# Performance work log

Hardware: AMD Instinct MI355X
Metric: run time of the kernel (lower is better)

Reference implementation:

```python
import jax, jax.numpy as jnp
import numpy as np

D_MODEL = 1024
N_HEADS = 16
HEAD_DIM = D_MODEL // N_HEADS


def setup_inputs() -> dict:
    key = jax.random.key(0)
    ks = jax.random.split(key, 6)
    s = 1.0 / np.sqrt(D_MODEL)
    x = jax.random.normal(ks[0], (4, 2048, D_MODEL), dtype=jnp.float32)
    Wq = jax.random.uniform(ks[1], (D_MODEL, D_MODEL), jnp.float32, -s, s)
    Wk = jax.random.uniform(ks[2], (D_MODEL, D_MODEL), jnp.float32, -s, s)
    Wv = jax.random.uniform(ks[3], (D_MODEL, D_MODEL), jnp.float32, -s, s)
    Wo = jax.random.uniform(ks[4], (D_MODEL, D_MODEL), jnp.float32, -s, s)
    bo = jax.random.uniform(ks[5], (D_MODEL,), jnp.float32, -s, s)
    return {"x": x, "Wq": Wq, "Wk": Wk, "Wv": Wv, "Wo": Wo, "bo": bo}


def reference(x, Wq, Wk, Wv, Wo, bo):
    B, S, _ = x.shape
    # nn.Linear: x @ W.T
    def proj(W):
        return (x @ W.T).reshape(B, S, N_HEADS, HEAD_DIM).transpose(0, 2, 1, 3)
    q = proj(Wq)  # [B,H,S,Dh]
    k = proj(Wk)
    v = proj(Wv)
    scores = jnp.einsum("bhqd,bhkd->bhqk", q, k) / jnp.sqrt(jnp.float32(HEAD_DIM))
    attn = jax.nn.softmax(scores, axis=-1)
    out = jnp.einsum("bhqk,bhkd->bhqd", attn, v)
    out = out.transpose(0, 2, 1, 3).reshape(B, S, D_MODEL)
    return out @ Wo.T + bo
```

## Files before the change

### kernel.cpp

```cpp
#include <hip/hip_runtime.h>
#include <hip/hip_bf16.h>
#include <math.h>

#define BB 4
#define SS 2048
#define DM 1024
#define NH 16
#define DH 64
#define MROWS (BB*SS)
#define NT (SS/64)

typedef __attribute__((ext_vector_type(8))) short bf16x8;
typedef __attribute__((ext_vector_type(4))) float f32x4;
typedef __attribute__((ext_vector_type(8))) unsigned short u16x8;

__device__ __forceinline__ unsigned short f2b(float f) {
    __hip_bfloat16 b = __float2bfloat16(f);
    return *reinterpret_cast<unsigned short*>(&b);
}

__device__ __forceinline__ float fexp2(float x) {
    float r;
    asm("v_exp_f32 %0, %1" : "=v"(r) : "v"(x));
    return r;
}

__device__ __forceinline__ void gload_lds16(const void* g, void* l) {
    __builtin_amdgcn_global_load_lds((const __attribute__((address_space(1))) unsigned int*)g,
                                     (__attribute__((address_space(3))) unsigned int*)l,
                                     16, 0, 0);
}

__global__ __launch_bounds__(256) void cast_x_kernel(const float* __restrict__ in,
                                                     unsigned short* __restrict__ out) {
    const size_t i = ((size_t)blockIdx.x * 256 + threadIdx.x) * 8;
    const float4 a = *(const float4*)(in + i);
    const float4 b = *(const float4*)(in + i + 4);
    unsigned short pk[8] = {f2b(a.x), f2b(a.y), f2b(a.z), f2b(a.w),
                            f2b(b.x), f2b(b.y), f2b(b.z), f2b(b.w)};
    *(u16x8*)(out + i) = *(u16x8*)pk;
}

__global__ __launch_bounds__(256) void cast_w_kernel(const float* __restrict__ Wq,
                                                     const float* __restrict__ Wk,
                                                     const float* __restrict__ Wv,
                                                     const float* __restrict__ Wo,
                                                     unsigned short* __restrict__ out) {
    const float* src = (blockIdx.y == 0) ? Wq : (blockIdx.y == 1) ? Wk
                     : (blockIdx.y == 2) ? Wv : Wo;
    const size_t i = ((size_t)blockIdx.x * 256 + threadIdx.x) * 8;
    const float4 a = *(const float4*)(src + i);
    const float4 b = *(const float4*)(src + i + 4);
    unsigned short pk[8] = {f2b(a.x), f2b(a.y), f2b(a.z), f2b(a.w),
                            f2b(b.x), f2b(b.y), f2b(b.z), f2b(b.w)};
    *(u16x8*)(out + (size_t)blockIdx.y * DM * DM + i) = *(u16x8*)pk;
}

template<int MODE>
__global__ __launch_bounds__(256) void gemm_mfma(const unsigned short* __restrict__ A,
                                                 const unsigned short* __restrict__ Wq,
                                                 const unsigned short* __restrict__ Wk,
                                                 const unsigned short* __restrict__ Wv,
                                                 unsigned short* __restrict__ Oq,
                                                 unsigned short* __restrict__ Ok,
                                                 unsigned short* __restrict__ Ov,
                                                 float* __restrict__ outf,
                                                 const float* __restrict__ bias) {
    __shared__ __align__(16) unsigned short As[128 * 64];
    __shared__ __align__(16) unsigned short Bs[128 * 64];
    const int t  = threadIdx.x;
    const int l  = t & 63;
    const int w  = t >> 6;
    const int g  = l >> 4;
    const int cc = l & 15;
    const int wr = w >> 1, wc = w & 1;
    const int m0 = blockIdx.x * 128;
    const int n0 = blockIdx.y * 128;

    const unsigned short* W;
    unsigned short* Ob = nullptr;
    float oscale = 1.f;
    if (MODE == 0) {
        const int z = blockIdx.z;
        W  = (z == 0) ? Wq : (z == 1) ? Wk : Wv;
        Ob = (z == 0) ? Oq : (z == 1) ? Ok : Ov;
        if (z == 0) oscale = 0.18033688011112042f;
    } else {
        W = Wq;
    }

    const f32x4 zf = {0.f, 0.f, 0.f, 0.f};
    f32x4 acc[4][4] = {{zf,zf,zf,zf},{zf,zf,zf,zf},{zf,zf,zf,zf},{zf,zf,zf,zf}};

    for (int k0 = 0; k0 < DM; k0 += 64) {
        __syncthreads();
        #pragma unroll
        for (int i = 0; i < 4; ++i) {
            const int s   = i * 256 + t;
            const int row = s >> 3;
            const int j   = s & 7;
            const int gb  = j ^ (row & 7);
            gload_lds16(A + (size_t)(m0 + row) * DM + k0 + gb * 8, &As[s * 8]);
            gload_lds16(W + (size_t)(n0 + row) * DM + k0 + gb * 8, &Bs[s * 8]);
        }
        asm volatile("s_waitcnt vmcnt(0)" ::: "memory");
        __syncthreads();

        #pragma unroll
        for (int kk = 0; kk < 2; ++kk) {
            bf16x8 af[4], bf[4];
            #pragma unroll
            for (int mi = 0; mi < 4; ++mi) {
                const int row = wr * 64 + mi * 16 + cc;
                const int jb  = (kk * 4 + g) ^ (row & 7);
                af[mi] = *(const bf16x8*)&As[(row * 8 + jb) * 8];
            }
            #pragma unroll
            for (int ni = 0; ni < 4; ++ni) {
                const int row = wc * 64 + ni * 16 + cc;
                const int jb  = (kk * 4 + g) ^ (row & 7);
                bf[ni] = *(const bf16x8*)&Bs[(row * 8 + jb) * 8];
            }
            #pragma unroll
            for (int mi = 0; mi < 4; ++mi)
                #pragma unroll
                for (int ni = 0; ni < 4; ++ni)
                    acc[mi][ni] = __builtin_amdgcn_mfma_f32_16x16x32_bf16(af[mi], bf[ni], acc[mi][ni], 0, 0, 0);
        }
    }

    #pragma unroll
    for (int mi = 0; mi < 4; ++mi) {
        #pragma unroll
        for (int r = 0; r < 4; ++r) {
            const int m = m0 + wr * 64 + mi * 16 + 4 * g + r;
            if (MODE == 0) {
                const int b = m >> 11, s = m & 2047;
                #pragma unroll
                for (int ni = 0; ni < 4; ++ni) {
                    const int col = n0 + wc * 64 + ni * 16 + cc;
                    const int h = col >> 6, dh = col & 63;
                    Ob[((size_t)(b * NH + h) * SS + s) * DH + dh] = f2b(acc[mi][ni][r] * oscale);
                }
            } else {
                #pragma unroll
                for (int ni = 0; ni < 4; ++ni) {
                    const int col = n0 + wc * 64 + ni * 16 + cc;
                    outf[(size_t)m * DM + col] = acc[mi][ni][r] + bias[col];
                }
            }
        }
    }
}

__global__ __launch_bounds__(256) void transpose_v(const unsigned short* __restrict__ Vb,
                                                   unsigned short* __restrict__ Vt) {
    __shared__ unsigned short T[64][72];
    const int t  = threadIdx.x;
    const int bh = blockIdx.y;
    const int s0 = blockIdx.x * 64;
    #pragma unroll
    for (int r = 0; r < 2; ++r) {
        const int idx = t + 256 * r;
        const int row = idx >> 3;
        const int d8  = (idx & 7) * 8;
        *(u16x8*)&T[row][d8] = *(const u16x8*)(Vb + ((size_t)bh * SS + s0 + row) * 64 + d8);
    }
    __syncthreads();
    const int d  = t >> 2;
    const int sc = (t & 3) * 16;
    unsigned short tmp[16];
    #pragma unroll
    for (int i = 0; i < 16; ++i) tmp[i] = T[sc + i][d];
    unsigned short* dst = Vt + ((size_t)bh * 64 + d) * SS + s0 + sc;
    *(u16x8*)(dst)     = *(u16x8*)&tmp[0];
    *(u16x8*)(dst + 8) = *(u16x8*)&tmp[8];
}

__global__ __launch_bounds__(256) void attn_mfma(const unsigned short* __restrict__ Qb,
                                                 const unsigned short* __restrict__ Kb,
                                                 const unsigned short* __restrict__ Vtp,
                                                 unsigned short* __restrict__ AOb) {
    __shared__ __align__(16) unsigned short Ks[2][64*64];
    __shared__ __align__(16) unsigned short Vs[2][64*64];
    __shared__ unsigned short Ps[64*64];
    const int t    = threadIdx.x;
    const int lane = t & 63;
    const int w    = t >> 6;
    const int g    = lane >> 4;
    const int cc   = lane & 15;
    const int bh   = blockIdx.y;
    const int q0   = blockIdx.x * 64;

    const unsigned short* Qw = Qb + ((size_t)bh * SS + q0 + w * 16 + cc) * 64;
    const bf16x8 qf0 = *(const bf16x8*)(Qw + 8 * g);
    const bf16x8 qf1 = *(const bf16x8*)(Qw + 32 + 8 * g);

    const unsigned short* Kbase = Kb  + (size_t)bh * SS * 64;
    const unsigned short* Vbase = Vtp + (size_t)bh * 64 * SS;

    auto stage = [&](int buf, int kt) {
        #pragma unroll
        for (int r2 = 0; r2 < 2; ++r2) {
            const int idx = r2 * 256 + t;
            const int row = idx >> 3;
            const int gb  = (idx & 7) ^ (row & 7);
            gload_lds16(Kbase + (size_t)(kt * 64 + row) * 64 + gb * 8, &Ks[buf][idx * 8]);
            gload_lds16(Vbase + (size_t)row * SS + kt * 64 + gb * 8, &Vs[buf][idx * 8]);
        }
    };

    asm volatile("s_waitcnt vmcnt(0)" ::: "memory");
    stage(0, 0);

    const f32x4 zf = {0.f, 0.f, 0.f, 0.f};
    f32x4 oacc[4] = {zf, zf, zf, zf};
    float mrow[4] = {-INFINITY, -INFINITY, -INFINITY, -INFINITY};
    float lrow[4] = {0.f, 0.f, 0.f, 0.f};

    for (int kt = 0; kt < NT; ++kt) {
        const int cur = kt & 1;
        if (kt + 1 < NT) {
            stage(cur ^ 1, kt + 1);
            asm volatile("s_waitcnt vmcnt(4)" ::: "memory");
        } else {
            asm volatile("s_waitcnt vmcnt(0)" ::: "memory");
        }
        __syncthreads();

        f32x4 sacc[4] = {zf, zf, zf, zf};
        __builtin_amdgcn_s_setprio(1);
        #pragma unroll
        for (int n = 0; n < 4; ++n) {
            const int key = n * 16 + cc;
            const bf16x8 kf0 = *(const bf16x8*)&Ks[cur][key * 64 + ((g       ^ (key & 7)) << 3)];
            const bf16x8 kf1 = *(const bf16x8*)&Ks[cur][key * 64 + (((4 + g) ^ (key & 7)) << 3)];
            sacc[n] = __builtin_amdgcn_mfma_f32_16x16x32_bf16(qf0, kf0, sacc[n], 0, 0, 0);
            sacc[n] = __builtin_amdgcn_mfma_f32_16x16x32_bf16(qf1, kf1, sacc[n], 0, 0, 0);
        }
        __builtin_amdgcn_s_setprio(0);

        float p[4][4];
        float scl[4];
        #pragma unroll
        for (int r = 0; r < 4; ++r) {
            float mx = fmaxf(fmaxf(sacc[0][r], sacc[1][r]), fmaxf(sacc[2][r], sacc[3][r]));
            mx = fmaxf(mx, __shfl_xor(mx, 1));
            mx = fmaxf(mx, __shfl_xor(mx, 2));
            mx = fmaxf(mx, __shfl_xor(mx, 4));
            mx = fmaxf(mx, __shfl_xor(mx, 8));
            const float nm = fmaxf(mrow[r], mx);
            scl[r] = fexp2(mrow[r] - nm);
            mrow[r] = nm;
            float rs = 0.f;
            #pragma unroll
            for (int n = 0; n < 4; ++n) {
                const float pv = fexp2(sacc[n][r] - nm);
                p[n][r] = pv;
                rs += pv;
            }
            rs += __shfl_xor(rs, 1);
            rs += __shfl_xor(rs, 2);
            rs += __shfl_xor(rs, 4);
            rs += __shfl_xor(rs, 8);
            lrow[r] = lrow[r] * scl[r] + rs;
        }

        #pragma unroll
        for (int n = 0; n < 4; ++n)
            #pragma unroll
            for (int r = 0; r < 4; ++r) {
                const int qr  = w * 16 + g * 4 + r;
                const int key = n * 16 + cc;
                Ps[qr * 64 + (key ^ ((qr & 7) << 3))] = f2b(p[n][r]);
            }

        #pragma unroll
        for (int n = 0; n < 4; ++n) {
            oacc[n][0] *= scl[0]; oacc[n][1] *= scl[1];
            oacc[n][2] *= scl[2]; oacc[n][3] *= scl[3];
        }

        const int qrow = w * 16 + cc;
        __builtin_amdgcn_s_setprio(1);
        #pragma unroll
        for (int ks = 0; ks < 2; ++ks) {
            const bf16x8 pf = *(const bf16x8*)&Ps[qrow * 64 + (((ks * 4 + g) ^ (qrow & 7)) << 3)];
            #pragma unroll
            for (int n = 0; n < 4; ++n) {
                const int vrow = n * 16 + cc;
                const bf16x8 vf = *(const bf16x8*)&Vs[cur][vrow * 64 + (((ks * 4 + g) ^ (vrow & 7)) << 3)];
                oacc[n] = __builtin_amdgcn_mfma_f32_16x16x32_bf16(pf, vf, oacc[n], 0, 0, 0);
            }
        }
        __builtin_amdgcn_s_setprio(0);

        __syncthreads();
    }

    const int b = bh >> 4, h = bh & 15;
    #pragma unroll
    for (int r = 0; r < 4; ++r) {
        const float inv  = 1.f / lrow[r];
        const int   srow = q0 + w * 16 + g * 4 + r;
        unsigned short* dst = AOb + ((size_t)(b * SS + srow)) * DM + h * 64;
        dst[ 0 + cc] = f2b(oacc[0][r] * inv);
        dst[16 + cc] = f2b(oacc[1][r] * inv);
        dst[32 + cc] = f2b(oacc[2][r] * inv);
        dst[48 + cc] = f2b(oacc[3][r] * inv);
    }
}

extern "C" void kernel_launch(void* const* d_in, const int* in_sizes, int n_in,
                              void* d_out, int out_size, void* d_ws, size_t ws_size,
                              hipStream_t stream) {
    const float* x  = (const float*)d_in[0];
    const float* Wq = (const float*)d_in[1];
    const float* Wk = (const float*)d_in[2];
    const float* Wv = (const float*)d_in[3];
    const float* Wo = (const float*)d_in[4];
    const float* bo = (const float*)d_in[5];
    float* out = (float*)d_out;

    const size_t NEL = (size_t)MROWS * DM;
    unsigned short* xb  = (unsigned short*)d_ws;
    unsigned short* Wb  = xb + NEL;
    unsigned short* Qb  = Wb + (size_t)4 * DM * DM;
    unsigned short* Kb  = Qb + NEL;
    unsigned short* Vb  = Kb + NEL;
    unsigned short* Vt  = Vb + NEL;
    unsigned short* AOb = Vt + NEL;

    const dim3 blk(256);
    cast_x_kernel<<<dim3(NEL / (256 * 8)), blk, 0, stream>>>(x, xb);
    cast_w_kernel<<<dim3(DM * DM / (256 * 8), 4), blk, 0, stream>>>(Wq, Wk, Wv, Wo, Wb);

    gemm_mfma<0><<<dim3(MROWS / 128, DM / 128, 3), blk, 0, stream>>>(
        xb, Wb, Wb + (size_t)DM * DM, Wb + (size_t)2 * DM * DM,
        Qb, Kb, Vb, nullptr, nullptr);

    transpose_v<<<dim3(SS / 64, BB * NH), blk, 0, stream>>>(Vb, Vt);
    attn_mfma<<<dim3(SS / 64, BB * NH), blk, 0, stream>>>(Qb, Kb, Vt, AOb);

    gemm_mfma<1><<<dim3(MROWS / 128, DM / 128, 1), blk, 0, stream>>>(
        AOb, Wb + (size_t)3 * DM * DM, nullptr, nullptr,
        nullptr, nullptr, nullptr, out, bo);
}
```

Baseline: 384.4 us.

## Transpose attention MFMA operands so each lane owns one query row

Swaps the A/B operands of the QK^T and PV MFMAs so the accumulator layout puts one query row per lane, with keys spread across the register index. Row max and row sum then need only two cross-lane shuffles instead of four per row, and mrow/lrow collapse to scalars. P is written to a per-wave LDS tile as packed 4-element stores with a new swizzle, and the output is written as vectorized 4-element stores. This cuts shuffle and scalar-store overhead in the softmax stage, at the cost of a new swizzle that has to stay bank-conflict free and layout-correct.

```diff
diff --git a/kernel.cpp b/kernel.cpp
--- a/kernel.cpp
+++ b/kernel.cpp
@@ -13,6 +13,7 @@
 typedef __attribute__((ext_vector_type(8))) short bf16x8;
 typedef __attribute__((ext_vector_type(4))) float f32x4;
 typedef __attribute__((ext_vector_type(8))) unsigned short u16x8;
+typedef __attribute__((ext_vector_type(4))) unsigned short u16x4;
 
 __device__ __forceinline__ unsigned short f2b(float f) {
     __hip_bfloat16 b = __float2bfloat16(f);
@@ -183,12 +184,13 @@
                                                  unsigned short* __restrict__ AOb) {
     __shared__ __align__(16) unsigned short Ks[2][64*64];
     __shared__ __align__(16) unsigned short Vs[2][64*64];
-    __shared__ unsigned short Ps[64*64];
+    __shared__ __align__(16) unsigned short Ps[4][16*64];
     const int t    = threadIdx.x;
     const int lane = t & 63;
     const int w    = t >> 6;
     const int g    = lane >> 4;
     const int cc   = lane & 15;
+    const int c7   = cc & 7;
     const int bh   = blockIdx.y;
     const int q0   = blockIdx.x * 64;
 
@@ -215,8 +217,9 @@
 
     const f32x4 zf = {0.f, 0.f, 0.f, 0.f};
     f32x4 oacc[4] = {zf, zf, zf, zf};
-    float mrow[4] = {-INFINITY, -INFINITY, -INFINITY, -INFINITY};
-    float lrow[4] = {0.f, 0.f, 0.f, 0.f};
+    float mrow = -INFINITY;
+    float lrow = 0.f;
+    unsigned short* Pw = &Ps[w][0];
 
     for (int kt = 0; kt < NT; ++kt) {
         const int cur = kt & 1;
@@ -235,62 +238,57 @@
             const int key = n * 16 + cc;
             const bf16x8 kf0 = *(const bf16x8*)&Ks[cur][key * 64 + ((g       ^ (key & 7)) << 3)];
             const bf16x8 kf1 = *(const bf16x8*)&Ks[cur][key * 64 + (((4 + g) ^ (key & 7)) << 3)];
-            sacc[n] = __builtin_amdgcn_mfma_f32_16x16x32_bf16(qf0, kf0, sacc[n], 0, 0, 0);
-            sacc[n] = __builtin_amdgcn_mfma_f32_16x16x32_bf16(qf1, kf1, sacc[n], 0, 0, 0);
+            sacc[n] = __builtin_amdgcn_mfma_f32_16x16x32_bf16(kf0, qf0, sacc[n], 0, 0, 0);
+            sacc[n] = __builtin_amdgcn_mfma_f32_16x16x32_bf16(kf1, qf1, sacc[n], 0, 0, 0);
         }
         __builtin_amdgcn_s_setprio(0);
 
+        float mx = fmaxf(fmaxf(sacc[0][0], sacc[0][1]), fmaxf(sacc[0][2], sacc[0][3]));
+        #pragma unroll
+        for (int n = 1; n < 4; ++n)
+            mx = fmaxf(mx, fmaxf(fmaxf(sacc[n][0], sacc[n][1]), fmaxf(sacc[n][2], sacc[n][3])));
+        mx = fmaxf(mx, __shfl_xor(mx, 16));
+        mx = fmaxf(mx, __shfl_xor(mx, 32));
+        const float nm  = fmaxf(mrow, mx);
+        const float scl = fexp2(mrow - nm);
+        mrow = nm;
+
         float p[4][4];
-        float scl[4];
-        #pragma unroll
-        for (int r = 0; r < 4; ++r) {
-            float mx = fmaxf(fmaxf(sacc[0][r], sacc[1][r]), fmaxf(sacc[2][r], sacc[3][r]));
-            mx = fmaxf(mx, __shfl_xor(mx, 1));
-            mx = fmaxf(mx, __shfl_xor(mx, 2));
-            mx = fmaxf(mx, __shfl_xor(mx, 4));
-            mx = fmaxf(mx, __shfl_xor(mx, 8));
-            const float nm = fmaxf(mrow[r], mx);
-            scl[r] = fexp2(mrow[r] - nm);
-            mrow[r] = nm;
-            float rs = 0.f;
-            #pragma unroll
-            for (int n = 0; n < 4; ++n) {
+        float rs = 0.f;
+        #pragma unroll
+        for (int n = 0; n < 4; ++n) {
+            #pragma unroll
+            for (int r = 0; r < 4; ++r) {
                 const float pv = fexp2(sacc[n][r] - nm);
                 p[n][r] = pv;
                 rs += pv;
             }
-            rs += __shfl_xor(rs, 1);
-            rs += __shfl_xor(rs, 2);
-            rs += __shfl_xor(rs, 4);
-            rs += __shfl_xor(rs, 8);
-            lrow[r] = lrow[r] * scl[r] + rs;
-        }
-
-        #pragma unroll
-        for (int n = 0; n < 4; ++n)
-            #pragma unroll
-            for (int r = 0; r < 4; ++r) {
-                const int qr  = w * 16 + g * 4 + r;
-                const int key = n * 16 + cc;
-                Ps[qr * 64 + (key ^ ((qr & 7) << 3))] = f2b(p[n][r]);
-            }
+        }
+        rs += __shfl_xor(rs, 16);
+        rs += __shfl_xor(rs, 32);
+        lrow = lrow * scl + rs;
 
         #pragma unroll
         for (int n = 0; n < 4; ++n) {
-            oacc[n][0] *= scl[0]; oacc[n][1] *= scl[1];
-            oacc[n][2] *= scl[2]; oacc[n][3] *= scl[3];
-        }
-
-        const int qrow = w * 16 + cc;
+            u16x4 pk = {f2b(p[n][0]), f2b(p[n][1]), f2b(p[n][2]), f2b(p[n][3])};
+            *(u16x4*)&Pw[cc * 64 + (((4 * n + g) ^ (2 * c7)) << 2)] = pk;
+        }
+
+        #pragma unroll
+        for (int n2 = 0; n2 < 4; ++n2) {
+            oacc[n2][0] *= scl; oacc[n2][1] *= scl;
+            oacc[n2][2] *= scl; oacc[n2][3] *= scl;
+        }
+
         __builtin_amdgcn_s_setprio(1);
         #pragma unroll
         for (int ks = 0; ks < 2; ++ks) {
-            const bf16x8 pf = *(const bf16x8*)&Ps[qrow * 64 + (((ks * 4 + g) ^ (qrow & 7)) << 3)];
-            #pragma unroll
-            for (int n = 0; n < 4; ++n) {
-                const int vrow = n * 16 + cc;
+            const bf16x8 pf = *(const bf16x8*)&Pw[cc * 64 + (((8 * ks + 2 * g) ^ (2 * c7)) << 2)];
+            #pragma unroll
+            for (int n2 = 0; n2 < 4; ++n2) {
+                const int vrow = n2 * 16 + cc;
                 const bf16x8 vf = *(const bf16x8*)&Vs[cur][vrow * 64 + (((ks * 4 + g) ^ (vrow & 7)) << 3)];
-                oacc[n] = __builtin_amdgcn_mfma_f32_16x16x32_bf16(pf, vf, oacc[n], 0, 0, 0);
+                oacc[n2] = __builtin_amdgcn_mfma_f32_16x16x32_bf16(vf, pf, oacc[n2], 0, 0, 0);
             }
         }
         __builtin_amdgcn_s_setprio(0);
@@ -299,15 +297,13 @@
     }
 
     const int b = bh >> 4, h = bh & 15;
+    const float inv = 1.f / lrow;
+    unsigned short* dst = AOb + ((size_t)(b * SS + q0 + w * 16 + cc)) * DM + h * 64;
     #pragma unroll
-    for (int r = 0; r < 4; ++r) {
-        const float inv  = 1.f / lrow[r];
-        const int   srow = q0 + w * 16 + g * 4 + r;
-        unsigned short* dst = AOb + ((size_t)(b * SS + srow)) * DM + h * 64;
-        dst[ 0 + cc] = f2b(oacc[0][r] * inv);
-        dst[16 + cc] = f2b(oacc[1][r] * inv);
-        dst[32 + cc] = f2b(oacc[2][r] * inv);
-        dst[48 + cc] = f2b(oacc[3][r] * inv);
+    for (int n2 = 0; n2 < 4; ++n2) {
+        u16x4 o = {f2b(oacc[n2][0] * inv), f2b(oacc[n2][1] * inv),
+                   f2b(oacc[n2][2] * inv), f2b(oacc[n2][3] * inv)};
+        *(u16x4*)(dst + n2 * 16 + 4 * g) = o;
     }
 }
 
```

Result: faster. 321.0 us (-16.5%).
